# Kernel optimization log

Measured on AMD Instinct MI355X. Metric: run time of the kernel, lower is better.

## Reference

```python
import jax, jax.numpy as jnp
import numpy as np

D, H, W = 40, 32, 88
BEV_H, BEV_W = 125, 125
X_MIN, X_MAX, DX = -50.0, 50.0, 0.8
Y_MIN, Y_MAX, DY = -50.0, 50.0, 0.8
Z_MIN, DZ = -10.0, 20.0


def _voxel_indices():
    """Replicates frustum creation + get_geometry + index computation.
    Returns (flat_idx, valid) each of shape (D, H, W). Faithful to the
    original's sequential in-place max() semantics."""
    # depth_grid = arange(1, 41, 1) + 1  -> 2..41
    depth = jnp.arange(1.0, 41.0, 1.0) + 1.0            # (D,)
    xs = jnp.linspace(0.0, W - 1.0, W)                  # (W,)
    ys = jnp.linspace(0.0, H - 1.0, H)                  # (H,)
    d = depth[:, None, None]                            # (D,1,1)
    xd = jnp.broadcast_to(xs[None, None, :] * d, (D, H, W))  # x*depth
    yd = jnp.broadcast_to(ys[None, :, None] * d, (D, H, W))  # y*depth
    zd = jnp.broadcast_to(d, (D, H, W))                       # depth
    # first points_d.max(): over columns (xd, yd, zd)
    max1 = jnp.maximum(xd.max(), jnp.maximum(yd.max(), zd.max()))
    gx = xd / max1 * (X_MAX - X_MIN) + X_MIN
    # second points_d.max(): column 0 was overwritten in-place by gx
    max2 = jnp.maximum(gx.max(), jnp.maximum(yd.max(), zd.max()))
    gy = yd / max2 * (Y_MAX - Y_MIN) + Y_MIN
    gz = zd
    # voxelize (torch .long() truncates; all values here are >= 0)
    ix = ((gx - X_MIN) / DX).astype(jnp.int32)
    iy = ((gy - Y_MIN) / DY).astype(jnp.int32)
    iz = ((gz - Z_MIN) / DZ).astype(jnp.int32)
    valid = (ix >= 0) & (ix < BEV_W) & (iy >= 0) & (iy < BEV_H) & (iz >= 0)
    flat_idx = jnp.where(valid, iy * BEV_W + ix, 0)
    return flat_idx, valid


def setup_inputs() -> dict:
    key = jax.random.key(0)
    k1, k2, k3, k4, k5 = jax.random.split(key, 5)
    B, N, C = 1, 6, 128
    return {
        "img_feat": jax.random.normal(k1, (B, N, C, H, W), dtype=jnp.float32),
        "depth_logits": jax.random.normal(k2, (B, N, D, H, W), dtype=jnp.float32),
        "rots": jax.random.normal(k3, (B, N, 3, 3), dtype=jnp.float32),
        "trans": jax.random.normal(k4, (B, N, 3), dtype=jnp.float32),
        "intrins": jax.random.normal(k5, (B, N, 3, 3), dtype=jnp.float32),
    }


def reference(img_feat, depth_logits, rots, trans, intrins):
    B, N, C, h, w = img_feat.shape
    depth_probs = jax.nn.softmax(depth_logits, axis=2)         # (B,N,D,H,W)
    # depth-weighted outer product: (B,N,D,H,W,C)
    feats = jnp.einsum('bnchw,bndhw->bndhwc', img_feat, depth_probs)
    flat_feats = feats.reshape(-1, C)                          # (B*N*D*H*W, C)
    flat_idx, valid = _voxel_indices()                         # (D,H,W)
    idx = jnp.broadcast_to(flat_idx[None, None], (B, N, D, h, w)).reshape(-1)
    msk = jnp.broadcast_to(valid[None, None], (B, N, D, h, w)).reshape(-1)
    flat_feats = jnp.where(msk[:, None], flat_feats, 0.0)
    bev = jax.ops.segment_sum(flat_feats, idx, num_segments=BEV_H * BEV_W)
    bev = bev.reshape(BEV_H, BEV_W, C)
    return jnp.transpose(bev, (2, 0, 1))[None]                 # (1, C, 125, 125)
```

## Files before the change

kernel.cpp:

```cpp
#include <hip/hip_runtime.h>


constexpr int D = 40, H = 32, W = 88, HW = H * W;
constexpr int C = 128, NCAM = 6;
constexpr int BEV = 125, NBINS = BEV * BEV;
constexpr int NCOLS = NCAM * HW;

typedef __attribute__((ext_vector_type(8))) unsigned short us8;
typedef __attribute__((ext_vector_type(4))) float f4;
typedef __attribute__((ext_vector_type(2))) float f2;

__device__ __forceinline__ unsigned short f2bf(float x) {
    unsigned u = __float_as_uint(x);
    return (unsigned short)((u + 0x7FFF + ((u >> 16) & 1)) >> 16);
}

struct Tabs { short XP[D][126]; short YP[D][126]; };
constexpr Tabs make_tabs() {
    Tabs t{};
    for (int d = 0; d < D; ++d) {
        int dep = d + 2;
        int cntx[126] = {};
        for (int w = 0; w < W; ++w) {
            float gx = (float)(w * dep) / 3567.0f * 100.0f - 50.0f;
            int ix = (int)((gx + 50.0f) / 0.8f);
            if (ix < 125) cntx[ix]++;
        }
        t.XP[d][0] = 0;
        for (int X = 0; X < 125; ++X) t.XP[d][X + 1] = (short)(t.XP[d][X] + cntx[X]);
        int cnty[126] = {};
        for (int h = 0; h < H; ++h) {
            float gy = (float)(h * dep) / 1271.0f * 100.0f - 50.0f;
            int iy = (int)((gy + 50.0f) / 0.8f);
            if (iy < 125) cnty[iy]++;
        }
        t.YP[d][0] = 0;
        for (int Y = 0; Y < 125; ++Y) t.YP[d][Y + 1] = (short)(t.YP[d][Y] + cnty[Y]);
    }
    return t;
}
constexpr Tabs g_tabs = make_tabs();
__device__ const Tabs g_tab = g_tabs;

struct SegTable { unsigned a[4096]; unsigned b[4096]; int n; };

constexpr SegTable make_segs() {
    SegTable S{};
    int ns = 0;
    for (int iy = 0; iy < 125; ++iy) {
        int cnt[125] = {};
        for (int d = 0; d < D; ++d) {
            int yc = g_tabs.YP[d][iy + 1] - g_tabs.YP[d][iy];
            if (yc == 0) continue;
            for (int X = 0; X < 125; ++X)
                cnt[X] += (g_tabs.XP[d][X + 1] - g_tabs.XP[d][X]) * yc;
        }
        int X = 0;
        while (X < 125) {
            if (cnt[X] > 176) {
                int d0 = 0;
                while (d0 < D) {
                    int run = 0, d1 = d0;
                    while (d1 < D) {
                        int piece = (g_tabs.XP[d1][X + 1] - g_tabs.XP[d1][X]) *
                                    (g_tabs.YP[d1][iy + 1] - g_tabs.YP[d1][iy]);
                        if (d1 > d0 && run + piece > 128) break;
                        run += piece; ++d1;
                    }
                    if (run > 0) {
                        S.a[ns] = ((unsigned)iy << 16) | ((unsigned)X << 8) | (unsigned)(X + 1);
                        S.b[ns] = (1u << 31) | ((unsigned)d0 << 25) | ((unsigned)d1 << 19) | (unsigned)run;
                        ++ns;
                    }
                    d0 = d1;
                }
                ++X;
            } else {
                int X0 = X, run = 0;
                while (X < 125 && (X - X0) < 16 && cnt[X] <= 176 &&
                       (X == X0 || run + cnt[X] <= 128)) {
                    run += cnt[X]; ++X;
                }
                if (run > 0) {
                    S.a[ns] = ((unsigned)iy << 16) | ((unsigned)X0 << 8) | (unsigned)X;
                    S.b[ns] = ((unsigned)0 << 25) | ((unsigned)D << 19) | (unsigned)run;
                    ++ns;
                }
            }
        }
    }
    S.n = ns;
    return S;
}
constexpr SegTable g_raw = make_segs();

constexpr SegTable reorder_segs() {
    SegTable R{};
    int pos = 0;
    for (int i = 0; i < g_raw.n; ++i)
        if ((int)(g_raw.b[i] & 0x7FFFF) >= 120) { R.a[pos] = g_raw.a[i]; R.b[pos] = g_raw.b[i]; ++pos; }
    for (int i = 0; i < g_raw.n; ++i)
        if ((int)(g_raw.b[i] & 0x7FFFF) <  120) { R.a[pos] = g_raw.a[i]; R.b[pos] = g_raw.b[i]; ++pos; }
    R.n = pos;
    return R;
}
constexpr SegTable g_ct = reorder_segs();
constexpr int NSEG = g_ct.n;
static_assert(NSEG > 0 && NSEG <= 4096, "seg table overflow");
__device__ const SegTable g_segs = g_ct;

struct Meta { unsigned m[4096]; int ne; };
constexpr Meta make_meta() {
    Meta M{};
    int pos = 0;
    for (int i = 0; i < NSEG; ++i) {
        int cnt = (int)(g_ct.b[i] & 0x7FFFF);
        int ng = (((cnt + 1) >> 1) + 3) >> 2;
        M.m[i] = (g_ct.b[i] & 0x80000000u) | ((unsigned)pos << 10) | (unsigned)ng;
        pos += 2 * ng * 4;
    }
    M.ne = pos;
    return M;
}
constexpr Meta g_mt = make_meta();
constexpr int NE_TOT = g_mt.ne;
static_assert(NE_TOT < (1 << 21), "start field overflow");
struct MetaArr { unsigned m[4096]; };
constexpr MetaArr make_meta_arr() { MetaArr A{}; for (int i = 0; i < 4096; ++i) A.m[i] = g_mt.m[i]; return A; }
__device__ const MetaArr g_metaD = make_meta_arr();

__device__ __align__(16) unsigned g_glist[NE_TOT + 64];

constexpr int SMAX_BLOCKS  = NCOLS / 256;
constexpr int BUILD_BLOCKS = (NSEG + 3) / 4;
constexpr int PACK_BLOCKS  = (C / 8) * (HW / 32);
constexpr int ZERO_TOTAL   = C * NBINS / 4;
constexpr int ZERO_BLOCKS  = (ZERO_TOTAL + 1023) / 1024;
constexpr int MEGA_BLOCKS  = SMAX_BLOCKS + BUILD_BLOCKS + PACK_BLOCKS + ZERO_BLOCKS;

__global__ void __launch_bounds__(256) mega_kernel(
        const float* __restrict__ feat,
        const float* __restrict__ logits,
        float* __restrict__ probs_t,
        unsigned short* __restrict__ feat_p,
        float* __restrict__ out) {
    __shared__ __align__(16) float tile[NCAM * 8 * 37];
    int b = blockIdx.x, t = threadIdx.x;

    if (b < SMAX_BLOCKS) {
        int col = b * 256 + t;
        int n  = col / HW;
        int hw = col - n * HW;
        const float* src = logits + ((size_t)n * D) * HW + hw;
        float m = -3.402823466e+38f;
#pragma unroll 20
        for (int d = 0; d < D; ++d)
            m = fmaxf(m, src[(size_t)d * HW]);
        float s = 0.f;
#pragma unroll 8
        for (int d = 0; d < D; ++d)
            s += expf(src[(size_t)d * HW] - m);
        float inv = 1.0f / s;
#pragma unroll 8
        for (int d = 0; d < D; ++d)
            probs_t[(size_t)((d << 12) | hw) * 8 + n] =
                expf(src[(size_t)d * HW] - m) * inv;

    } else if (b < SMAX_BLOCKS + BUILD_BLOCKS) {
        int slot = (b - SMAX_BLOCKS) * 4 + (t >> 6);
        int lane = t & 63;
        if (slot < NSEG) {
            unsigned da = g_segs.a[slot], db = g_segs.b[slot], mb = g_metaD.m[slot];
            int iy = (int)(da >> 16), X0 = (int)((da >> 8) & 0xFF), X1 = (int)(da & 0xFF);
            int d0 = (int)((db >> 25) & 0x3F), d1 = (int)((db >> 19) & 0x3F);
            int drange = d1 - d0;
            int ng4 = (int)(mb & 0x3FFu) * 4;
            unsigned* gl = g_glist + ((mb >> 10) & 0x1FFFFFu);
            int base = 0;
            for (int bl = 0; bl < X1 - X0; ++bl) {
                int d = d0 + lane;
                int hb = 0, he = 0, wb = 0, we = 0, cnt = 0;
                if (lane < drange) {
                    hb = g_tab.YP[d][iy];      he = g_tab.YP[d][iy + 1];
                    wb = g_tab.XP[d][X0 + bl]; we = g_tab.XP[d][X0 + bl + 1];
                    cnt = (he - hb) * (we - wb);
                }
                int inc = cnt;
#pragma unroll
                for (int delta = 1; delta < 64; delta <<= 1) {
                    int y = __shfl_up(inc, delta, 64);
                    if (lane >= delta) inc += y;
                }
                int tot = __shfl(inc, 63, 64);
                int o = base + inc - cnt;
                int run_end = base + tot;
                for (int h = hb; h < he; ++h)
                    for (int w = wb; w < we; ++w) {
                        unsigned v = ((unsigned)bl << 19) | ((unsigned)d << 12)
                                   | (unsigned)(h * W + w);
                        if (o >= run_end - 2) v |= 0x80000000u;
                        gl[(o & 1) * ng4 + (o >> 1)] = v;
                        ++o;
                    }
                base = run_end;
            }
            int m = base;
#pragma unroll
            for (int dg = 0; dg < 2; ++dg) {
                int cnt2 = (m + 1 - dg) >> 1;
                for (int k = cnt2 + lane; k < ng4; k += 64)
                    gl[dg * ng4 + k] = (16u << 19) | 0x80000000u;
            }
        }

    } else if (b < SMAX_BLOCKS + BUILD_BLOCKS + PACK_BLOCKS) {
        int bb = b - SMAX_BLOCKS - BUILD_BLOCKS;
        int c0  = (bb / 88) * 8;
        int hw0 = (bb % 88) * 32;
        int cq = t >> 5, hwL = t & 31;
#pragma unroll
        for (int n = 0; n < NCAM; ++n)
            tile[(n * 8 + cq) * 37 + hwL] =
                feat[((size_t)(n * C + c0 + cq)) * HW + hw0 + hwL];
        __syncthreads();
        int hl = t >> 3, cL = t & 7;
        unsigned short v[6];
#pragma unroll
        for (int n = 0; n < NCAM; ++n)
            v[n] = f2bf(tile[(n * 8 + cL) * 37 + hl]);
        unsigned* dst = (unsigned*)(feat_p +
            ((size_t)(hw0 + hl) * C + (c0 + cL)) * 6);
        dst[0] = (unsigned)v[0] | ((unsigned)v[1] << 16);
        dst[1] = (unsigned)v[2] | ((unsigned)v[3] << 16);
        dst[2] = (unsigned)v[4] | ((unsigned)v[5] << 16);

    } else {
        int base = (b - SMAX_BLOCKS - BUILD_BLOCKS - PACK_BLOCKS) * 1024;
#pragma unroll
        for (int k = 0; k < 4; ++k) {
            int i = base + k * 256 + t;
            if (i < ZERO_TOTAL) ((f4*)out)[i] = f4{0.f, 0.f, 0.f, 0.f};
        }
    }
}

__global__ void __launch_bounds__(128, 2) gather_kernel(
        const unsigned short* __restrict__ feat_p,
        const float* __restrict__ probs_t,
        float* __restrict__ out) {
    __shared__ __align__(16) float T[2][17][66];
    __shared__ __align__(16) unsigned EL[192];
    int t = threadIdx.x;
    int slot = blockIdx.x >> 1, chalf = blockIdx.x & 1;
    unsigned da = g_segs.a[slot], mb = g_metaD.m[slot];
    int iy = (int)(da >> 16), X0 = (int)((da >> 8) & 0xFF), X1 = (int)(da & 0xFF);
    int width = X1 - X0;
    bool split = (mb >> 31) != 0;
    int ng = (int)(mb & 0x3FFu);
    unsigned start = (mb >> 10) & 0x1FFFFFu;
    int dg = __builtin_amdgcn_readfirstlane((int)(threadIdx.x >> 6));
    int lane = t & 63;
    int c = chalf * 64 + lane;
    int ntot = ng * 8;

    if (t < ntot) EL[t] = g_glist[start + (unsigned)t];
    if (t + 128 < ntot) EL[t + 128] = g_glist[start + (unsigned)(t + 128)];
    { float* Tf = &T[0][0][0];
      for (int i = t; i < 2 * 17 * 66; i += 128) Tf[i] = 0.f; }
    __syncthreads();

    const unsigned* ep = EL + dg * ng * 4;
    const char* fbase = (const char*)feat_p + (size_t)c * 12;
    float* Tp = &T[dg][0][0];
    float racc = 0.f;

#define LOADE(E, g_) { uint4 ee_ = *(const uint4*)(ep + 4 * (g_));            \
    E[0] = (unsigned)__builtin_amdgcn_readfirstlane((int)ee_.x);              \
    E[1] = (unsigned)__builtin_amdgcn_readfirstlane((int)ee_.y);              \
    E[2] = (unsigned)__builtin_amdgcn_readfirstlane((int)ee_.z);              \
    E[3] = (unsigned)__builtin_amdgcn_readfirstlane((int)ee_.w); }
#define ISSUE(S, E) _Pragma("unroll") for (int i_ = 0; i_ < 4; ++i_) {        \
    const unsigned* fp_ = (const unsigned*)(fbase +                           \
                          (size_t)(E[i_] & 0xFFFu) * 1536);                   \
    fv##S[i_][0] = fp_[0]; fv##S[i_][1] = fp_[1]; fv##S[i_][2] = fp_[2];      \
    const float* pp_ = probs_t + ((size_t)(E[i_] & 0x3FFFFu) << 3);           \
    pa##S[i_] = *(const f4*)pp_; pb##S[i_] = *(const f2*)(pp_ + 4); }
#define CONS(S, E) _Pragma("unroll") for (int i_ = 0; i_ < 4; ++i_) {         \
    unsigned u0_ = fv##S[i_][0], u1_ = fv##S[i_][1], u2_ = fv##S[i_][2];      \
    racc += pa##S[i_].x * __uint_as_float(u0_ << 16)                          \
          + pa##S[i_].y * __uint_as_float(u0_ & 0xFFFF0000u)                  \
          + pa##S[i_].z * __uint_as_float(u1_ << 16)                          \
          + pa##S[i_].w * __uint_as_float(u1_ & 0xFFFF0000u)                  \
          + pb##S[i_].x * __uint_as_float(u2_ << 16)                          \
          + pb##S[i_].y * __uint_as_float(u2_ & 0xFFFF0000u);                 \
    if (E[i_] & 0x80000000u) {                                                \
        Tp[((E[i_] >> 19) & 31u) * 66 + (unsigned)lane] += racc; racc = 0.f; } }

    unsigned EA[4], EB[4], EC[4];
    unsigned fvA[4][3], fvB[4][3], fvC[4][3];
    f4 paA[4], paB[4], paC[4];
    f2 pbA[4], pbB[4], pbC[4];
    LOADE(EA, 0); ISSUE(A, EA);
    LOADE(EB, 1); ISSUE(B, EB);
    LOADE(EC, 2);
    int g = 0;
    for (; g + 3 <= ng; g += 3) {
        ISSUE(C, EC);
        CONS(A, EA);
        LOADE(EA, g + 3); ISSUE(A, EA);
        CONS(B, EB);
        LOADE(EB, g + 4); ISSUE(B, EB);
        CONS(C, EC);
        LOADE(EC, g + 5);
    }
    if (g + 2 < ng) ISSUE(C, EC);
    if (g     < ng) CONS(A, EA);
    if (g + 1 < ng) CONS(B, EB);
    if (g + 2 < ng) CONS(C, EC);
#undef LOADE
#undef ISSUE
#undef CONS
    __syncthreads();

    int binbase = iy * BEV + X0;
#pragma unroll
    for (int it = 0; it < 8; ++it) {
        int bl = t & 15, cc = it * 8 + (t >> 4);
        if (bl < width) {
            float v = T[0][bl][cc] + T[1][bl][cc];
            float* dst = &out[(size_t)(chalf * 64 + cc) * NBINS + binbase + bl];
            if (split) atomicAdd(dst, v);
            else       *dst = v;
        }
    }
}

extern "C" void kernel_launch(void* const* d_in, const int* in_sizes, int n_in,
                              void* d_out, int out_size, void* d_ws, size_t ws_size,
                              hipStream_t stream) {
    const float* img_feat     = (const float*)d_in[0];
    const float* depth_logits = (const float*)d_in[1];
    float* out = (float*)d_out;

    char* p = (char*)d_ws;
    float*          probs_t = (float*)p;          p += (size_t)D * 4096 * 8 * 4;
    unsigned short* feat_p  = (unsigned short*)p; p += (size_t)HW * C * 6 * 2;

    mega_kernel<<<MEGA_BLOCKS, 256, 0, stream>>>(
        img_feat, depth_logits, probs_t, feat_p, out);
    gather_kernel<<<NSEG * 2, 128, 0, stream>>>(feat_p, probs_t, out);
}
```

Baseline: 106.3 us.

## Coalesce softmax output via shared staging and merge channel halves per gather block

The softmax blocks now cover 42 pixel columns across all 6 cameras. Probabilities are staged in shared memory so each pixel's 6 camera values go out as one 16-byte plus one 8-byte store, replacing scattered 4-byte stores. Build blocks are moved to the front of the mega kernel. The gather kernel now runs one 256-thread block per segment covering both channel halves, so the entry list is loaded once rather than twice. The cost is extra barriers in the softmax path and more shared memory and registers per gather block, which may lower occupancy.

Result: faster. 103.8 us (-2.3%).

```diff
diff --git a/kernel.cpp b/kernel.cpp
--- a/kernel.cpp
+++ b/kernel.cpp
@@ -131,12 +131,13 @@
 
 __device__ __align__(16) unsigned g_glist[NE_TOT + 64];
 
-constexpr int SMAX_BLOCKS  = NCOLS / 256;
+constexpr int SMAX_HWT    = 42;
+constexpr int SMAX_BLOCKS = (HW + SMAX_HWT - 1) / SMAX_HWT;
 constexpr int BUILD_BLOCKS = (NSEG + 3) / 4;
 constexpr int PACK_BLOCKS  = (C / 8) * (HW / 32);
 constexpr int ZERO_TOTAL   = C * NBINS / 4;
 constexpr int ZERO_BLOCKS  = (ZERO_TOTAL + 1023) / 1024;
-constexpr int MEGA_BLOCKS  = SMAX_BLOCKS + BUILD_BLOCKS + PACK_BLOCKS + ZERO_BLOCKS;
+constexpr int MEGA_BLOCKS  = BUILD_BLOCKS + SMAX_BLOCKS + PACK_BLOCKS + ZERO_BLOCKS;
 
 __global__ void __launch_bounds__(256) mega_kernel(
         const float* __restrict__ feat,
@@ -144,30 +145,11 @@
         float* __restrict__ probs_t,
         unsigned short* __restrict__ feat_p,
         float* __restrict__ out) {
-    __shared__ __align__(16) float tile[NCAM * 8 * 37];
+    __shared__ __align__(16) float shmem[2016];
     int b = blockIdx.x, t = threadIdx.x;
 
-    if (b < SMAX_BLOCKS) {
-        int col = b * 256 + t;
-        int n  = col / HW;
-        int hw = col - n * HW;
-        const float* src = logits + ((size_t)n * D) * HW + hw;
-        float m = -3.402823466e+38f;
-#pragma unroll 20
-        for (int d = 0; d < D; ++d)
-            m = fmaxf(m, src[(size_t)d * HW]);
-        float s = 0.f;
-#pragma unroll 8
-        for (int d = 0; d < D; ++d)
-            s += expf(src[(size_t)d * HW] - m);
-        float inv = 1.0f / s;
-#pragma unroll 8
-        for (int d = 0; d < D; ++d)
-            probs_t[(size_t)((d << 12) | hw) * 8 + n] =
-                expf(src[(size_t)d * HW] - m) * inv;
-
-    } else if (b < SMAX_BLOCKS + BUILD_BLOCKS) {
-        int slot = (b - SMAX_BLOCKS) * 4 + (t >> 6);
+    if (b < BUILD_BLOCKS) {
+        int slot = b * 4 + (t >> 6);
         int lane = t & 63;
         if (slot < NSEG) {
             unsigned da = g_segs.a[slot], db = g_segs.b[slot], mb = g_metaD.m[slot];
@@ -213,21 +195,63 @@
             }
         }
 
-    } else if (b < SMAX_BLOCKS + BUILD_BLOCKS + PACK_BLOCKS) {
-        int bb = b - SMAX_BLOCKS - BUILD_BLOCKS;
+    } else if (b < BUILD_BLOCKS + SMAX_BLOCKS) {
+        int hw0 = (b - BUILD_BLOCKS) * SMAX_HWT;
+        int n   = t / SMAX_HWT;
+        int hwL = t - n * SMAX_HWT;
+        int hw  = hw0 + hwL;
+        bool act = (n < NCAM) && (hw < HW);
+        const float* src = logits + ((size_t)n * D) * HW + hw;
+        float m = -3.402823466e+38f, inv = 0.f;
+        if (act) {
+#pragma unroll 20
+            for (int d = 0; d < D; ++d)
+                m = fmaxf(m, src[(size_t)d * HW]);
+            float s = 0.f;
+#pragma unroll 8
+            for (int d = 0; d < D; ++d)
+                s += expf(src[(size_t)d * HW] - m);
+            inv = 1.0f / s;
+        }
+        for (int dc = 0; dc < D; dc += 8) {
+            if (act) {
+#pragma unroll
+                for (int j = 0; j < 8; ++j)
+                    shmem[(j * NCAM + n) * SMAX_HWT + hwL] =
+                        expf(src[(size_t)(dc + j) * HW] - m) * inv;
+            }
+            __syncthreads();
+            for (int cell = t; cell < 8 * SMAX_HWT; cell += 256) {
+                int j = cell / SMAX_HWT, hl = cell - j * SMAX_HWT;
+                if (hw0 + hl < HW) {
+                    const float* ps = &shmem[(j * NCAM) * SMAX_HWT + hl];
+                    f4 lo = { ps[0], ps[SMAX_HWT], ps[2 * SMAX_HWT], ps[3 * SMAX_HWT] };
+                    f2 hi = { ps[4 * SMAX_HWT], ps[5 * SMAX_HWT] };
+                    float* dst = probs_t +
+                        ((size_t)(((dc + j) << 12) | (hw0 + hl)) << 3);
+                    *(f4*)dst = lo;
+                    *(f2*)(dst + 4) = hi;
+                }
+            }
+            __syncthreads();
+        }
+
+    } else if (b < BUILD_BLOCKS + SMAX_BLOCKS + PACK_BLOCKS) {
+        float* tile = shmem;
+        int bb = b - BUILD_BLOCKS - SMAX_BLOCKS;
         int c0  = (bb / 88) * 8;
         int hw0 = (bb % 88) * 32;
         int cq = t >> 5, hwL = t & 31;
 #pragma unroll
-        for (int n = 0; n < NCAM; ++n)
-            tile[(n * 8 + cq) * 37 + hwL] =
-                feat[((size_t)(n * C + c0 + cq)) * HW + hw0 + hwL];
+        for (int n2 = 0; n2 < NCAM; ++n2)
+            tile[(n2 * 8 + cq) * 37 + hwL] =
+                feat[((size_t)(n2 * C + c0 + cq)) * HW + hw0 + hwL];
         __syncthreads();
         int hl = t >> 3, cL = t & 7;
         unsigned short v[6];
 #pragma unroll
-        for (int n = 0; n < NCAM; ++n)
-            v[n] = f2bf(tile[(n * 8 + cL) * 37 + hl]);
+        for (int n2 = 0; n2 < NCAM; ++n2)
+            v[n2] = f2bf(tile[(n2 * 8 + cL) * 37 + hl]);
         unsigned* dst = (unsigned*)(feat_p +
             ((size_t)(hw0 + hl) * C + (c0 + cL)) * 6);
         dst[0] = (unsigned)v[0] | ((unsigned)v[1] << 16);
@@ -235,7 +259,7 @@
         dst[2] = (unsigned)v[4] | ((unsigned)v[5] << 16);
 
     } else {
-        int base = (b - SMAX_BLOCKS - BUILD_BLOCKS - PACK_BLOCKS) * 1024;
+        int base = (b - BUILD_BLOCKS - SMAX_BLOCKS - PACK_BLOCKS) * 1024;
 #pragma unroll
         for (int k = 0; k < 4; ++k) {
             int i = base + k * 256 + t;
@@ -244,34 +268,35 @@
     }
 }
 
-__global__ void __launch_bounds__(128, 2) gather_kernel(
+__global__ void __launch_bounds__(256, 2) gather_kernel(
         const unsigned short* __restrict__ feat_p,
         const float* __restrict__ probs_t,
         float* __restrict__ out) {
-    __shared__ __align__(16) float T[2][17][66];
+    __shared__ __align__(16) float T[2][2][17][66];
     __shared__ __align__(16) unsigned EL[192];
     int t = threadIdx.x;
-    int slot = blockIdx.x >> 1, chalf = blockIdx.x & 1;
+    int slot = blockIdx.x;
     unsigned da = g_segs.a[slot], mb = g_metaD.m[slot];
     int iy = (int)(da >> 16), X0 = (int)((da >> 8) & 0xFF), X1 = (int)(da & 0xFF);
     int width = X1 - X0;
     bool split = (mb >> 31) != 0;
     int ng = (int)(mb & 0x3FFu);
     unsigned start = (mb >> 10) & 0x1FFFFFu;
-    int dg = __builtin_amdgcn_readfirstlane((int)(threadIdx.x >> 6));
+    int wave  = __builtin_amdgcn_readfirstlane((int)(threadIdx.x >> 6));
+    int dg    = wave & 1;
+    int chalf = wave >> 1;
     int lane = t & 63;
     int c = chalf * 64 + lane;
     int ntot = ng * 8;
 
     if (t < ntot) EL[t] = g_glist[start + (unsigned)t];
-    if (t + 128 < ntot) EL[t + 128] = g_glist[start + (unsigned)(t + 128)];
-    { float* Tf = &T[0][0][0];
-      for (int i = t; i < 2 * 17 * 66; i += 128) Tf[i] = 0.f; }
+    { float* Tf = &T[0][0][0][0];
+      for (int i = t; i < 2 * 2 * 17 * 66; i += 256) Tf[i] = 0.f; }
     __syncthreads();
 
     const unsigned* ep = EL + dg * ng * 4;
     const char* fbase = (const char*)feat_p + (size_t)c * 12;
-    float* Tp = &T[dg][0][0];
+    float* Tp = &T[dg][chalf][0][0];
     float racc = 0.f;
 
 #define LOADE(E, g_) { uint4 ee_ = *(const uint4*)(ep + 4 * (g_));            \
@@ -325,10 +350,11 @@
     int binbase = iy * BEV + X0;
 #pragma unroll
     for (int it = 0; it < 8; ++it) {
-        int bl = t & 15, cc = it * 8 + (t >> 4);
+        int bl = t & 15, cc = it * 16 + (t >> 4);
         if (bl < width) {
-            float v = T[0][bl][cc] + T[1][bl][cc];
-            float* dst = &out[(size_t)(chalf * 64 + cc) * NBINS + binbase + bl];
+            int ch = cc >> 6, cl = cc & 63;
+            float v = T[0][ch][bl][cl] + T[1][ch][bl][cl];
+            float* dst = &out[(size_t)cc * NBINS + binbase + bl];
             if (split) atomicAdd(dst, v);
             else       *dst = v;
         }
@@ -348,5 +374,5 @@
 
     mega_kernel<<<MEGA_BLOCKS, 256, 0, stream>>>(
         img_feat, depth_logits, probs_t, feat_p, out);
-    gather_kernel<<<NSEG * 2, 128, 0, stream>>>(feat_p, probs_t, out);
-}
+    gather_kernel<<<NSEG, 256, 0, stream>>>(feat_p, probs_t, out);
+}
```
